# Performance work log

Hardware: AMD Instinct MI355X
Metric: run time of the kernel (lower is better)

Reference implementation:

```python
import jax, jax.numpy as jnp
import numpy as np

B, D_MODEL, N_LAYERS = 8, 512, 4
D_STATE, D_CONV, EXPAND, DT_RANK = 16, 4, 2, 32
D_INNER = EXPAND * D_MODEL
NUM_CLASSES = 10
ALPHA = 0.2  # observer_alpha
LN_EPS = 1e-5


def setup_inputs() -> dict:
    key = jax.random.key(0)
    ks = jax.random.split(key, 10)
    std = 0.02
    rn = lambda k, sh: (jax.random.normal(k, sh) * std).astype(jnp.float32)
    return {
        "x": jax.random.normal(ks[0], (B, 3, 32, 32), dtype=jnp.float32),
        "W_inp": rn(ks[1], (3, D_MODEL)), "b_inp": jnp.zeros((D_MODEL,), jnp.float32),
        "W_in": rn(ks[2], (N_LAYERS, D_MODEL, 2 * D_INNER)), "b_in": jnp.zeros((N_LAYERS, 2 * D_INNER), jnp.float32),
        "conv_w": rn(ks[3], (N_LAYERS, D_INNER, D_CONV)), "conv_b": jnp.zeros((N_LAYERS, D_INNER), jnp.float32),
        "W_x": rn(ks[4], (N_LAYERS, D_INNER, DT_RANK + 2 * D_STATE)),
        "W_dt": rn(ks[5], (N_LAYERS, DT_RANK, D_INNER)), "b_dt": jnp.zeros((N_LAYERS, D_INNER), jnp.float32),
        "A_log": jnp.broadcast_to(jnp.log(jnp.arange(1, D_STATE + 1, dtype=jnp.float32)), (N_LAYERS, D_INNER, D_STATE)) + 0.0,
        "D_skip": jnp.ones((N_LAYERS, D_INNER), jnp.float32),
        "W_out": rn(ks[6], (N_LAYERS, D_INNER, D_MODEL)), "b_out": jnp.zeros((N_LAYERS, D_MODEL), jnp.float32),
        "ln_w": jnp.ones((N_LAYERS, D_MODEL), jnp.float32), "ln_b": jnp.zeros((N_LAYERS, D_MODEL), jnp.float32),
        "lnf_w": jnp.ones((D_MODEL,), jnp.float32), "lnf_b": jnp.zeros((D_MODEL,), jnp.float32),
        "W_cls": rn(ks[7], (D_MODEL, NUM_CLASSES)), "b_cls": jnp.zeros((NUM_CLASSES,), jnp.float32),
    }


def layernorm(x, w, b):
    mu = x.mean(-1, keepdims=True)
    var = jnp.mean(jnp.square(x - mu), -1, keepdims=True)
    return (x - mu) * jax.lax.rsqrt(var + LN_EPS) * w + b


def mamba_layer(x, Wi, bi, cw, cb, Wx, Wdt, bdt, Alog, Dv, Wo, bo):
    # x: [B, L, d_model]
    Bsz, L, _ = x.shape
    u, z = jnp.split(x @ Wi + bi, 2, axis=-1)  # each [B, L, d_inner]
    # causal depthwise conv1d, kernel width D_CONV
    up = jnp.pad(u, ((0, 0), (D_CONV - 1, 0), (0, 0)))
    uc = cb + sum(up[:, k:k + L, :] * cw[:, k] for k in range(D_CONV))
    uc = jax.nn.silu(uc)
    dbc = uc @ Wx  # [B, L, dt_rank + 2*d_state]
    dt = jax.nn.softplus(dbc[..., :DT_RANK] @ Wdt + bdt)       # [B, L, d_inner]
    Bm = dbc[..., DT_RANK:DT_RANK + D_STATE]                    # [B, L, d_state]
    Cm = dbc[..., DT_RANK + D_STATE:]                           # [B, L, d_state]
    A = -jnp.exp(Alog)                                          # [d_inner, d_state]

    def step(h, inp):
        u_t, dt_t, B_t, C_t = inp  # [B,E],[B,E],[B,N],[B,N]
        h = jnp.exp(dt_t[..., None] * A) * h + (dt_t * u_t)[..., None] * B_t[:, None, :]
        # Luenberger observer correction: h <- h + alpha * (u - C.h) * C^T
        err = u_t - jnp.einsum('ben,bn->be', h, C_t)
        h = h + ALPHA * err[..., None] * C_t[:, None, :]
        y = jnp.einsum('ben,bn->be', h, C_t)
        return h, y

    step = jax.checkpoint(step)
    h0 = jnp.zeros((Bsz, D_INNER, D_STATE), dtype=x.dtype)
    xs = (uc.transpose(1, 0, 2), dt.transpose(1, 0, 2), Bm.transpose(1, 0, 2), Cm.transpose(1, 0, 2))
    _, ys = jax.lax.scan(step, h0, xs)
    y = ys.transpose(1, 0, 2) + Dv * uc
    y = y * jax.nn.silu(z)
    return y @ Wo + bo


def reference(x, W_inp, b_inp, W_in, b_in, conv_w, conv_b, W_x, W_dt, b_dt, A_log, D_skip, W_out, b_out, ln_w, ln_b, lnf_w, lnf_b, W_cls, b_cls):
    Bsz = x.shape[0]
    t = x.transpose(0, 2, 3, 1).reshape(Bsz, -1, 3)  # [B, H*W, 3]
    t = t @ W_inp + b_inp                             # [B, L, d_model]
    for i in range(N_LAYERS):
        t = t + mamba_layer(layernorm(t, ln_w[i], ln_b[i]), W_in[i], b_in[i], conv_w[i], conv_b[i], W_x[i], W_dt[i], b_dt[i], A_log[i], D_skip[i], W_out[i], b_out[i])
    t = t.mean(axis=1)
    t = layernorm(t, lnf_w, lnf_b)
    return t @ W_cls + b_cls
```

## Files before the change

kernel.cpp:

```cpp
#include <hip/hip_runtime.h>
#include <hip/hip_bf16.h>
#include <math.h>

#define BSZ 8
#define SEQL 1024
#define DM 512
#define DI 1024
#define DST 16
#define DTR 32
#define NLAYERS 4
#define ALPHA_C 0.2f
#define LNEPS 1e-5f
#define CH 64
#define KS64 8
#define YSTR 18

typedef __attribute__((ext_vector_type(8))) short short8;
typedef __attribute__((ext_vector_type(4))) float f32x4;

__device__ __forceinline__ void gll16(const void* g, void* l) {
    __builtin_amdgcn_global_load_lds(
        (const __attribute__((address_space(1))) unsigned int*)g,
        (__attribute__((address_space(3))) unsigned int*)l, 16, 0, 0);
}

__device__ __forceinline__ float sum16(float x) {
    x += __int_as_float(__builtin_amdgcn_update_dpp(0, __float_as_int(x), 0x121, 0xf, 0xf, true));
    x += __int_as_float(__builtin_amdgcn_update_dpp(0, __float_as_int(x), 0x122, 0xf, 0xf, true));
    x += __int_as_float(__builtin_amdgcn_update_dpp(0, __float_as_int(x), 0x124, 0xf, 0xf, true));
    x += __int_as_float(__builtin_amdgcn_update_dpp(0, __float_as_int(x), 0x128, 0xf, 0xf, true));
    return x;
}

__device__ __forceinline__ float bf2f(unsigned short v) {
    return __uint_as_float(((unsigned)v) << 16);
}

__global__ __launch_bounds__(256) void embed_kernel(const float* __restrict__ x,
                                                    const float* __restrict__ Wi,
                                                    const float* __restrict__ bi,
                                                    float* __restrict__ t) {
    int idx = blockIdx.x * 256 + threadIdx.x;
    if (idx >= BSZ * SEQL * DM) return;
    int d  = idx & (DM - 1);
    int bl = idx >> 9;
    int l  = bl & (SEQL - 1);
    int b  = bl >> 10;
    const float* xb = x + (size_t)b * 3 * SEQL;
    float acc = bi[d];
    acc += xb[0 * SEQL + l] * Wi[0 * DM + d];
    acc += xb[1 * SEQL + l] * Wi[1 * DM + d];
    acc += xb[2 * SEQL + l] * Wi[2 * DM + d];
    t[idx] = acc;
}

__global__ __launch_bounds__(256) void ln_kernel(const float* __restrict__ t,
                                                 const float* __restrict__ w,
                                                 const float* __restrict__ b,
                                                 __hip_bfloat16* __restrict__ xn) {
    int row = blockIdx.x;
    int tid = threadIdx.x;
    const float* r = t + (size_t)row * DM;
    float v0 = r[tid], v1 = r[tid + 256];
    __shared__ float sh[256], sh2[256];
    sh[tid]  = v0 + v1;
    sh2[tid] = v0 * v0 + v1 * v1;
    __syncthreads();
    for (int off = 128; off > 0; off >>= 1) {
        if (tid < off) { sh[tid] += sh[tid + off]; sh2[tid] += sh2[tid + off]; }
        __syncthreads();
    }
    float mu  = sh[0]  * (1.f / DM);
    float var = sh2[0] * (1.f / DM) - mu * mu;
    float rs  = rsqrtf(var + LNEPS);
    xn[(size_t)row * DM + tid]       = __float2bfloat16((v0 - mu) * rs * w[tid]       + b[tid]);
    xn[(size_t)row * DM + tid + 256] = __float2bfloat16((v1 - mu) * rs * w[tid + 256] + b[tid + 256]);
}

__global__ __launch_bounds__(256) void transpose_bf_kernel(const float* __restrict__ W,
                                                           __hip_bfloat16* __restrict__ Wt,
                                                           int K, int N, size_t lstride) {
    const float* Wl = W + (size_t)blockIdx.z * lstride;
    __hip_bfloat16* Wtl = Wt + (size_t)blockIdx.z * lstride;
    __shared__ float tile[32][33];
    int kk = blockIdx.x * 32, nn = blockIdx.y * 32;
    int tx = threadIdx.x & 31, ty = threadIdx.x >> 5;
#pragma unroll
    for (int i = 0; i < 32; i += 8)
        tile[ty + i][tx] = Wl[(size_t)(kk + ty + i) * N + nn + tx];
    __syncthreads();
#pragma unroll
    for (int i = 0; i < 32; i += 8)
        Wtl[(size_t)(nn + ty + i) * K + kk + tx] = __float2bfloat16(tile[tx][ty + i]);
}

template <int OUTMODE>
__global__ __launch_bounds__(256) void gemm_mfma_kernel(const short* __restrict__ A,
                                                        const short* __restrict__ Bt,
                                                        const float* __restrict__ bias,
                                                        void* __restrict__ Cv,
                                                        int M, int N, int K) {
    __shared__ __align__(16) short As[128 * 32];
    __shared__ __align__(16) short Bs[128 * 32];
    int tid = threadIdx.x;
    int w = tid >> 6, lane = tid & 63;
    int quad = lane >> 4, ml = lane & 15;
    int wm = w & 1, wn = w >> 1;
    const short* Ab = A + (size_t)blockIdx.x * 128 * K;
    const short* Bb = Bt + (size_t)blockIdx.y * 128 * K;
    f32x4 acc[4][4] = {};
    int s0 = tid, s1 = tid + 256;
    int r0 = s0 >> 2, c0 = (s0 & 3) ^ ((r0 >> 1) & 3);
    int r1 = s1 >> 2, c1 = (s1 & 3) ^ ((r1 >> 1) & 3);
    int aoff[4], boff[4];
#pragma unroll
    for (int t = 0; t < 4; t++) {
        int ra = wm * 64 + t * 16 + ml;
        aoff[t] = ra * 32 + (quad ^ ((ra >> 1) & 3)) * 8;
        int rb = wn * 64 + t * 16 + ml;
        boff[t] = rb * 32 + (quad ^ ((rb >> 1) & 3)) * 8;
    }
    for (int kk = 0; kk < K; kk += 32) {
        gll16(Ab + (size_t)r0 * K + kk + c0 * 8, As + (size_t)(w * 64) * 8);
        gll16(Ab + (size_t)r1 * K + kk + c1 * 8, As + (size_t)(256 + w * 64) * 8);
        gll16(Bb + (size_t)r0 * K + kk + c0 * 8, Bs + (size_t)(w * 64) * 8);
        gll16(Bb + (size_t)r1 * K + kk + c1 * 8, Bs + (size_t)(256 + w * 64) * 8);
        __syncthreads();
        short8 af[4], bfr[4];
#pragma unroll
        for (int t = 0; t < 4; t++) af[t]  = *(const short8*)&As[aoff[t]];
#pragma unroll
        for (int t = 0; t < 4; t++) bfr[t] = *(const short8*)&Bs[boff[t]];
#pragma unroll
        for (int mt = 0; mt < 4; mt++)
#pragma unroll
            for (int nt = 0; nt < 4; nt++)
                acc[mt][nt] = __builtin_amdgcn_mfma_f32_16x16x32_bf16(af[mt], bfr[nt], acc[mt][nt], 0, 0, 0);
        __syncthreads();
    }
#pragma unroll
    for (int mt = 0; mt < 4; mt++) {
#pragma unroll
        for (int nt = 0; nt < 4; nt++) {
            int n = blockIdx.y * 128 + wn * 64 + nt * 16 + ml;
            float bv = bias[n];
#pragma unroll
            for (int r = 0; r < 4; r++) {
                int m = blockIdx.x * 128 + wm * 64 + mt * 16 + quad * 4 + r;
                size_t off = (size_t)m * N + n;
                float v = acc[mt][nt][r] + bv;
                if (OUTMODE == 2) {
                    ((unsigned short*)Cv)[off] = __bfloat16_as_ushort(__float2bfloat16(v));
                } else {
                    float* C = (float*)Cv;
                    if (OUTMODE == 1) v += C[off];
                    C[off] = v;
                }
            }
        }
    }
}

__global__ __launch_bounds__(256) void conv_kernel(const unsigned short* __restrict__ uzb,
                                                   const float* __restrict__ cw,
                                                   const float* __restrict__ cb,
                                                   unsigned short* __restrict__ ucb) {
    int idx = blockIdx.x * 256 + threadIdx.x;
    int e  = idx & (DI - 1);
    int bl = idx >> 10;
    int l  = bl & (SEQL - 1);
    int b  = bl >> 10;
    const unsigned short* u = uzb + (size_t)b * SEQL * 2048;
    float acc = cb[e];
#pragma unroll
    for (int k = 0; k < 4; k++) {
        int ll = l - 3 + k;
        float uv = (ll >= 0) ? bf2f(u[(size_t)ll * 2048 + e]) : 0.f;
        acc += uv * cw[e * 4 + k];
    }
    acc = acc / (1.f + __expf(-acc));
    ucb[idx] = __bfloat16_as_ushort(__float2bfloat16(acc));
}

__global__ __launch_bounds__(256) void gemm64_mfma_kernel(const short* __restrict__ A,
                                                          const short* __restrict__ Bt,
                                                          float* __restrict__ part,
                                                          int M) {
    const int K = DI;
    const int Kseg = K / KS64;
    __shared__ __align__(16) short As[128 * 32];
    __shared__ __align__(16) short Bs[64 * 32];
    int tid = threadIdx.x;
    int w = tid >> 6, lane = tid & 63;
    int quad = lane >> 4, ml = lane & 15;
    int wm = w & 1, wn = w >> 1;
    int bm = blockIdx.x, ks = blockIdx.y;
    const short* Ab = A + (size_t)bm * 128 * K;
    f32x4 acc[4][2] = {};
    int s0 = tid, s1 = tid + 256;
    int r0 = s0 >> 2, c0 = (s0 & 3) ^ ((r0 >> 1) & 3);
    int r1 = s1 >> 2, c1 = (s1 & 3) ^ ((r1 >> 1) & 3);
    int rB = tid >> 2, cB = (tid & 3) ^ ((rB >> 1) & 3);
    int aoff[4], boff[2];
#pragma unroll
    for (int t = 0; t < 4; t++) {
        int ra = wm * 64 + t * 16 + ml;
        aoff[t] = ra * 32 + (quad ^ ((ra >> 1) & 3)) * 8;
    }
#pragma unroll
    for (int t = 0; t < 2; t++) {
        int rb = wn * 32 + t * 16 + ml;
        boff[t] = rb * 32 + (quad ^ ((rb >> 1) & 3)) * 8;
    }
    int k0 = ks * Kseg;
    for (int kk = k0; kk < k0 + Kseg; kk += 32) {
        gll16(Ab + (size_t)r0 * K + kk + c0 * 8, As + (size_t)(w * 64) * 8);
        gll16(Ab + (size_t)r1 * K + kk + c1 * 8, As + (size_t)(256 + w * 64) * 8);
        gll16(Bt + (size_t)rB * K + kk + cB * 8, Bs + (size_t)(w * 64) * 8);
        __syncthreads();
        short8 af[4], bfr[2];
#pragma unroll
        for (int t = 0; t < 4; t++) af[t]  = *(const short8*)&As[aoff[t]];
#pragma unroll
        for (int t = 0; t < 2; t++) bfr[t] = *(const short8*)&Bs[boff[t]];
#pragma unroll
        for (int mt = 0; mt < 4; mt++)
#pragma unroll
            for (int nt = 0; nt < 2; nt++)
                acc[mt][nt] = __builtin_amdgcn_mfma_f32_16x16x32_bf16(af[mt], bfr[nt], acc[mt][nt], 0, 0, 0);
        __syncthreads();
    }
#pragma unroll
    for (int mt = 0; mt < 4; mt++) {
#pragma unroll
        for (int nt = 0; nt < 2; nt++) {
            int n = wn * 32 + nt * 16 + ml;
#pragma unroll
            for (int r = 0; r < 4; r++) {
                int m = bm * 128 + wm * 64 + mt * 16 + quad * 4 + r;
                part[((size_t)ks * M + m) * 64 + n] = acc[mt][nt][r];
            }
        }
    }
}

__global__ __launch_bounds__(256) void repack_kernel(const float* __restrict__ part,
                                                     float* __restrict__ dtc,
                                                     unsigned* __restrict__ bcb,
                                                     float* __restrict__ ssqb,
                                                     int M) {
    int m = blockIdx.x * 4 + (threadIdx.x >> 6);
    int j = threadIdx.x & 63;
    float v = 0.f;
#pragma unroll
    for (int ks = 0; ks < KS64; ks++) v += part[((size_t)ks * M + m) * 64 + j];
    if (j < 32) {
        dtc[(size_t)m * 32 + j] = v;
    } else {
        int n = (j - 32) & 15;
        unsigned short u16 = __bfloat16_as_ushort(__float2bfloat16(v));
        unsigned short* bp = (unsigned short*)(bcb + (size_t)m * 16 + n);
        if (j < 48) {
            bp[0] = u16;
        } else {
            bp[1] = u16;
            float vr = bf2f(u16);
            float s = sum16(vr * vr);
            if (j == 48) ssqb[m] = s;
        }
    }
}

__global__ __launch_bounds__(256) void dt_kernel(const float* __restrict__ dtc,
                                                 const float* __restrict__ Wdt,
                                                 const float* __restrict__ bdt,
                                                 float* __restrict__ dtb) {
    __shared__ float sdtc[32][32];
    __shared__ float swdt[32][256];
    int tid = threadIdx.x;
    int e0 = (blockIdx.x & 3) * 256;
    int m0 = (blockIdx.x >> 2) * 32;
#pragma unroll
    for (int i = 0; i < 4; i++) {
        int idx = tid + 256 * i;
        sdtc[idx >> 5][idx & 31] = dtc[(size_t)(m0 + (idx >> 5)) * 32 + (idx & 31)];
    }
#pragma unroll
    for (int r = 0; r < 32; r++) swdt[r][tid] = Wdt[(size_t)r * DI + e0 + tid];
    __syncthreads();
    float wc[32];
#pragma unroll
    for (int r = 0; r < 32; r++) wc[r] = swdt[r][tid];
    float bv = bdt[e0 + tid];
    for (int m = 0; m < 32; m++) {
        float acc = bv;
#pragma unroll
        for (int r4 = 0; r4 < 8; r4++) {
            float4 d4 = *(const float4*)&sdtc[m][r4 * 4];
            acc = fmaf(d4.x, wc[r4 * 4 + 0], acc);
            acc = fmaf(d4.y, wc[r4 * 4 + 1], acc);
            acc = fmaf(d4.z, wc[r4 * 4 + 2], acc);
            acc = fmaf(d4.w, wc[r4 * 4 + 3], acc);
        }
        float sp = (acc > 20.f) ? acc : log1pf(__expf(acc));
        dtb[(size_t)(m0 + m) * DI + e0 + tid] = sp;
    }
}

__device__ __forceinline__ void scan_stage(unsigned* sBC, float* sDT, unsigned short* sU,
                                           unsigned short* sZ, float* sSQ,
                                           const unsigned short* __restrict__ ucb_row,
                                           const float* __restrict__ dtb_row,
                                           const unsigned short* __restrict__ uzb_row,
                                           const unsigned* __restrict__ bcb_row,
                                           const float* __restrict__ sqb,
                                           int e_base, int tid, int tc) {
    int w = tid >> 6;
    gll16(bcb_row + (size_t)(tc + (tid >> 2)) * 16 + (tid & 3) * 4, sBC + w * 256);
    gll16(dtb_row + (size_t)(tc + (tid >> 2)) * 1024 + e_base + (tid & 3) * 4, sDT + w * 256);
    if (w < 2) {
        int t = tid >> 1, half = tid & 1;
        gll16(ucb_row + (size_t)(tc + t) * 1024 + e_base + half * 8, sU + w * 512);
        if (tid < 16) gll16(sqb + tc + tid * 4, sSQ);
    } else {
        int j = tid - 128;
        int t = j >> 1, half = j & 1;
        gll16(uzb_row + (size_t)(tc + t) * 2048 + 1024 + e_base + half * 8, sZ + (w - 2) * 512);
    }
}

__device__ __forceinline__ void scan_flush(const float* yb, __hip_bfloat16* ob,
                                           int e_base, int tcp, int tid) {
#pragma unroll
    for (int r = 0; r < 2; r++) {
        int pid = r * 256 + tid;
        int t = pid >> 3, ep = pid & 7;
        float2 y2 = *(const float2*)&yb[t * YSTR + ep * 2];
        __hip_bfloat162 v;
        v.x = __float2bfloat16(y2.x);
        v.y = __float2bfloat16(y2.y);
        *(__hip_bfloat162*)&ob[(size_t)(tcp + t) * DI + e_base + ep * 2] = v;
    }
}

__global__ __launch_bounds__(256) void scan_kernel(const unsigned short* __restrict__ ucb,
                                                   const float* __restrict__ dtb,
                                                   const unsigned short* __restrict__ uzb,
                                                   const unsigned* __restrict__ bcb,
                                                   const float* __restrict__ ssqb,
                                                   const float* __restrict__ Alog,
                                                   const float* __restrict__ Dv,
                                                   __hip_bfloat16* __restrict__ out) {
    __shared__ __align__(16) unsigned       sBC[2][CH * 16];
    __shared__ __align__(16) float          sDT[2][CH * 16];
    __shared__ __align__(16) unsigned short sU [2][CH * 16];
    __shared__ __align__(16) unsigned short sZ [2][CH * 16];
    __shared__ __align__(16) float          sSQ[2][CH];
    __shared__ __align__(16) float          yb [2][CH * YSTR];
    int tid = threadIdx.x;
    int g = tid >> 4, n = tid & 15;
    int b = blockIdx.x >> 6;
    int e_base = (blockIdx.x & 63) << 4;
    int e = e_base + g;
    float An2 = -__expf(Alog[e * DST + n]) * 1.4426950408889634f;
    float dv = Dv[e];
    const unsigned short* ucb_row = ucb + (size_t)b * SEQL * DI;
    const float*          dtb_row = dtb + (size_t)b * SEQL * DI;
    const unsigned short* uzb_row = uzb + (size_t)b * SEQL * 2048;
    const unsigned*       bcb_row = bcb + (size_t)b * SEQL * 16;
    const float*          sqb     = ssqb + (size_t)b * SEQL;
    __hip_bfloat16* ob = out + (size_t)b * SEQL * DI;
    float h = 0.f;
    scan_stage(sBC[0], sDT[0], sU[0], sZ[0], sSQ[0], ucb_row, dtb_row, uzb_row, bcb_row, sqb, e_base, tid, 0);
    int buf = 0;
    for (int c = 0; c < SEQL / CH; c++) {
        int tc = c * CH;
        __syncthreads();
        if (c + 1 < SEQL / CH)
            scan_stage(sBC[buf ^ 1], sDT[buf ^ 1], sU[buf ^ 1], sZ[buf ^ 1], sSQ[buf ^ 1],
                       ucb_row, dtb_row, uzb_row, bcb_row, sqb, e_base, tid, tc + CH);
        if (c > 0)
            scan_flush(yb[buf ^ 1], ob, e_base, tc - CH, tid);
        const unsigned* pBC = sBC[buf];
        const float* pDT = sDT[buf];
        const unsigned short* pU = sU[buf];
        const unsigned short* pZ = sZ[buf];
        const float* pSQ = sSQ[buf];
        float* pY = yb[buf];
        for (int ts = 0; ts < CH; ts += 16) {
            float pc = 0.f, ucap = 0.f;
#pragma unroll
            for (int j = 0; j < 16; j++) {
                int t = ts + j;
                unsigned bcd = pBC[t * 16 + n];
                float Bn = __uint_as_float(bcd << 16);
                float Cn = __uint_as_float(bcd & 0xFFFF0000u);
                float dtv = pDT[t * 16 + g];
                float uv  = bf2f(pU[t * 16 + g]);
                float alC = ALPHA_C * Cn;
                float a = __builtin_amdgcn_exp2f(dtv * An2);
                h = fmaf(a, h, dtv * uv * Bn);
                float p = sum16(h * Cn);
                h = fmaf(uv - p, alC, h);
                bool cap = (n == j);
                pc   = cap ? p  : pc;
                ucap = cap ? uv : ucap;
            }
            int tl = ts + n;
            float sq = pSQ[tl];
            float zv = bf2f(pZ[tl * 16 + g]);
            float es2 = ALPHA_C * (ucap - pc);
            float y = fmaf(dv, ucap, fmaf(es2, sq, pc));
            float sz = zv / (1.f + __expf(-zv));
            pY[tl * YSTR + g] = y * sz;
        }
        buf ^= 1;
    }
    __syncthreads();
    scan_flush(yb[buf ^ 1], ob, e_base, SEQL - CH, tid);
}

__global__ __launch_bounds__(512) void pool_kernel(const float* __restrict__ t,
                                                   float* __restrict__ part) {
    int b = blockIdx.x >> 4;
    int c = blockIdx.x & 15;
    int d = threadIdx.x;
    const float* tb = t + ((size_t)b * SEQL + c * 64) * DM + d;
    float s = 0.f;
    for (int l = 0; l < 64; l++) s += tb[(size_t)l * DM];
    part[(size_t)blockIdx.x * DM + d] = s;
}

__global__ __launch_bounds__(512) void final_kernel(const float* __restrict__ part,
                                                    const float* __restrict__ lw,
                                                    const float* __restrict__ lb,
                                                    const float* __restrict__ Wc,
                                                    const float* __restrict__ bc,
                                                    float* __restrict__ out) {
    int b = blockIdx.x;
    int d = threadIdx.x;
    float v = 0.f;
    for (int c = 0; c < 16; c++) v += part[((size_t)b * 16 + c) * DM + d];
    v *= (1.f / SEQL);
    __shared__ float sh[512], sh2[512], nd[512];
    sh[d] = v; sh2[d] = v * v;
    __syncthreads();
    for (int off = 256; off > 0; off >>= 1) {
        if (d < off) { sh[d] += sh[d + off]; sh2[d] += sh2[d + off]; }
        __syncthreads();
    }
    float mu  = sh[0]  * (1.f / DM);
    float var = sh2[0] * (1.f / DM) - mu * mu;
    float rs  = rsqrtf(var + LNEPS);
    nd[d] = (v - mu) * rs * lw[d] + lb[d];
    __syncthreads();
    if (d < 10) {
        float acc = bc[d];
        for (int k = 0; k < DM; k++) acc += nd[k] * Wc[k * 10 + d];
        out[b * 10 + d] = acc;
    }
}

extern "C" void kernel_launch(void* const* d_in, const int* in_sizes, int n_in,
                              void* d_out, int out_size, void* d_ws, size_t ws_size,
                              hipStream_t stream) {
    const float* x      = (const float*)d_in[0];
    const float* W_inp  = (const float*)d_in[1];
    const float* b_inp  = (const float*)d_in[2];
    const float* W_in   = (const float*)d_in[3];
    const float* b_in   = (const float*)d_in[4];
    const float* conv_w = (const float*)d_in[5];
    const float* conv_b = (const float*)d_in[6];
    const float* W_x    = (const float*)d_in[7];
    const float* W_dt   = (const float*)d_in[8];
    const float* b_dt   = (const float*)d_in[9];
    const float* A_log  = (const float*)d_in[10];
    const float* D_skip = (const float*)d_in[11];
    const float* W_out  = (const float*)d_in[12];
    const float* b_out  = (const float*)d_in[13];
    const float* ln_w   = (const float*)d_in[14];
    const float* ln_b   = (const float*)d_in[15];
    const float* lnf_w  = (const float*)d_in[16];
    const float* lnf_b  = (const float*)d_in[17];
    const float* W_cls  = (const float*)d_in[18];
    const float* b_cls  = (const float*)d_in[19];

    const int M = BSZ * SEQL;

    float* ws = (float*)d_ws;
    float* t_buf = ws;                    ws += (size_t)M * DM;
    unsigned short* uzb = (unsigned short*)ws;  ws += (size_t)M * 2048 / 2;
    unsigned short* ucb = (unsigned short*)ws;  ws += (size_t)M * DI / 2;
    float* dtb   = ws;                    ws += (size_t)M * DI;
    float* dtc   = ws;                    ws += (size_t)M * 32;
    unsigned* bcbu = (unsigned*)ws;       ws += (size_t)M * 16;
    float* ssqb  = ws;                    ws += (size_t)M;
    unsigned short* xn_bf = (unsigned short*)ws;  ws += (size_t)M * DM / 2;
    unsigned short* ucs_bf = (unsigned short*)ws; ws += (size_t)M * DI / 2;
    float* partb = ws;                    ws += (size_t)KS64 * M * 64;
    unsigned short* wtin_bf  = (unsigned short*)ws; ws += (size_t)NLAYERS * DM * 2048 / 2;
    unsigned short* wtout_bf = (unsigned short*)ws; ws += (size_t)NLAYERS * DI * DM / 2;
    unsigned short* wxt_bf   = (unsigned short*)ws; ws += (size_t)NLAYERS * DI * 64 / 2 + 64;
    float* poolp = ws;                    ws += (size_t)128 * DM;

    embed_kernel<<<(M * DM + 255) / 256, 256, 0, stream>>>(x, W_inp, b_inp, t_buf);
    transpose_bf_kernel<<<dim3(DM / 32, 2048 / 32, NLAYERS), 256, 0, stream>>>(
        W_in, (__hip_bfloat16*)wtin_bf, DM, 2048, (size_t)DM * 2048);
    transpose_bf_kernel<<<dim3(DI / 32, DM / 32, NLAYERS), 256, 0, stream>>>(
        W_out, (__hip_bfloat16*)wtout_bf, DI, DM, (size_t)DI * DM);
    transpose_bf_kernel<<<dim3(DI / 32, 64 / 32, NLAYERS), 256, 0, stream>>>(
        W_x, (__hip_bfloat16*)wxt_bf, DI, 64, (size_t)DI * 64);

    for (int i = 0; i < NLAYERS; i++) {
        ln_kernel<<<M, 256, 0, stream>>>(t_buf, ln_w + i * DM, ln_b + i * DM,
                                         (__hip_bfloat16*)xn_bf);
        gemm_mfma_kernel<2><<<dim3(M / 128, 2048 / 128), 256, 0, stream>>>(
            (const short*)xn_bf, (const short*)(wtin_bf + (size_t)i * DM * 2048),
            b_in + i * 2048, uzb, M, 2048, DM);
        conv_kernel<<<(M * DI) / 256, 256, 0, stream>>>(
            uzb, conv_w + (size_t)i * DI * 4, conv_b + i * DI, ucb);
        gemm64_mfma_kernel<<<dim3(M / 128, KS64), 256, 0, stream>>>(
            (const short*)ucb, (const short*)(wxt_bf + (size_t)i * DI * 64), partb, M);
        repack_kernel<<<M / 4, 256, 0, stream>>>(partb, dtc, bcbu, ssqb, M);
        dt_kernel<<<(M / 32) * 4, 256, 0, stream>>>(
            dtc, W_dt + (size_t)i * DTR * DI, b_dt + i * DI, dtb);
        scan_kernel<<<BSZ * DI / 16, 256, 0, stream>>>(
            ucb, dtb, uzb, bcbu, ssqb, A_log + (size_t)i * DI * DST, D_skip + i * DI,
            (__hip_bfloat16*)ucs_bf);
        gemm_mfma_kernel<1><<<dim3(M / 128, DM / 128), 256, 0, stream>>>(
            (const short*)ucs_bf, (const short*)(wtout_bf + (size_t)i * DI * DM),
            b_out + i * DM, t_buf, M, DM, DI);
    }

    pool_kernel<<<128, 512, 0, stream>>>(t_buf, poolp);
    final_kernel<<<8, 512, 0, stream>>>(poolp, lnf_w, lnf_b, W_cls, b_cls, (float*)d_out);
}
```

Measured before the change: 1.216 ms.

## Pack dt and u into bf16 pairs for scan, fold dt reduction, smaller out-proj tiles

The dt kernel now reduces the split-K partials itself and writes dt (as bf16) packed together with u into one 32-bit word per element. This replaces the separate fp32 dt buffer and bf16 u stream, so the scan kernel makes fewer global loads and uses less shared memory. z and the ssq values are now read directly from global memory inside the scan loop. The output projection uses a new 64x64-tile GEMM to launch more blocks for the N=512 residual GEMM. Rounding dt to bf16 adds precision risk, and the smaller tiles reduce data reuse per block.

```diff
diff --git a/kernel.cpp b/kernel.cpp
--- a/kernel.cpp
+++ b/kernel.cpp
@@ -156,6 +156,61 @@
                     if (OUTMODE == 1) v += C[off];
                     C[off] = v;
                 }
+            }
+        }
+    }
+}
+
+__global__ __launch_bounds__(256) void gemm6464_res_kernel(const short* __restrict__ A,
+                                                           const short* __restrict__ Bt,
+                                                           const float* __restrict__ bias,
+                                                           float* __restrict__ C,
+                                                           int M, int N, int K) {
+    __shared__ __align__(16) short As[64 * 32];
+    __shared__ __align__(16) short Bs[64 * 32];
+    int tid = threadIdx.x;
+    int w = tid >> 6, lane = tid & 63;
+    int quad = lane >> 4, ml = lane & 15;
+    int wm = w & 1, wn = w >> 1;
+    const short* Ab = A + (size_t)blockIdx.x * 64 * K;
+    const short* Bb = Bt + (size_t)blockIdx.y * 64 * K;
+    f32x4 acc[2][2] = {};
+    int r0 = tid >> 2, c0 = (tid & 3) ^ ((r0 >> 1) & 3);
+    int aoff[2], boff[2];
+#pragma unroll
+    for (int t = 0; t < 2; t++) {
+        int ra = wm * 32 + t * 16 + ml;
+        aoff[t] = ra * 32 + (quad ^ ((ra >> 1) & 3)) * 8;
+        int rb = wn * 32 + t * 16 + ml;
+        boff[t] = rb * 32 + (quad ^ ((rb >> 1) & 3)) * 8;
+    }
+    for (int kk = 0; kk < K; kk += 32) {
+        gll16(Ab + (size_t)r0 * K + kk + c0 * 8, As + (size_t)(w * 64) * 8);
+        gll16(Bb + (size_t)r0 * K + kk + c0 * 8, Bs + (size_t)(w * 64) * 8);
+        __syncthreads();
+        short8 af[2], bfr[2];
+#pragma unroll
+        for (int t = 0; t < 2; t++) af[t]  = *(const short8*)&As[aoff[t]];
+#pragma unroll
+        for (int t = 0; t < 2; t++) bfr[t] = *(const short8*)&Bs[boff[t]];
+#pragma unroll
+        for (int mt = 0; mt < 2; mt++)
+#pragma unroll
+            for (int nt = 0; nt < 2; nt++)
+                acc[mt][nt] = __builtin_amdgcn_mfma_f32_16x16x32_bf16(af[mt], bfr[nt], acc[mt][nt], 0, 0, 0);
+        __syncthreads();
+    }
+#pragma unroll
+    for (int mt = 0; mt < 2; mt++) {
+#pragma unroll
+        for (int nt = 0; nt < 2; nt++) {
+            int n = blockIdx.y * 64 + wn * 32 + nt * 16 + ml;
+            float bv = bias[n];
+#pragma unroll
+            for (int r = 0; r < 4; r++) {
+                int m = blockIdx.x * 64 + wm * 32 + mt * 16 + quad * 4 + r;
+                size_t off = (size_t)m * N + n;
+                C[off] = acc[mt][nt][r] + bv + C[off];
             }
         }
     }
@@ -245,36 +300,33 @@
 }
 
 __global__ __launch_bounds__(256) void repack_kernel(const float* __restrict__ part,
-                                                     float* __restrict__ dtc,
                                                      unsigned* __restrict__ bcb,
                                                      float* __restrict__ ssqb,
                                                      int M) {
-    int m = blockIdx.x * 4 + (threadIdx.x >> 6);
-    int j = threadIdx.x & 63;
+    int m = blockIdx.x * 8 + (threadIdx.x >> 5);
+    int j = threadIdx.x & 31;
     float v = 0.f;
 #pragma unroll
-    for (int ks = 0; ks < KS64; ks++) v += part[((size_t)ks * M + m) * 64 + j];
-    if (j < 32) {
-        dtc[(size_t)m * 32 + j] = v;
+    for (int ks = 0; ks < KS64; ks++) v += part[((size_t)ks * M + m) * 64 + 32 + j];
+    int n = j & 15;
+    unsigned short u16 = __bfloat16_as_ushort(__float2bfloat16(v));
+    unsigned short* bp = (unsigned short*)(bcb + (size_t)m * 16 + n);
+    if (j < 16) {
+        bp[0] = u16;
     } else {
-        int n = (j - 32) & 15;
-        unsigned short u16 = __bfloat16_as_ushort(__float2bfloat16(v));
-        unsigned short* bp = (unsigned short*)(bcb + (size_t)m * 16 + n);
-        if (j < 48) {
-            bp[0] = u16;
-        } else {
-            bp[1] = u16;
-            float vr = bf2f(u16);
-            float s = sum16(vr * vr);
-            if (j == 48) ssqb[m] = s;
-        }
-    }
-}
-
-__global__ __launch_bounds__(256) void dt_kernel(const float* __restrict__ dtc,
+        bp[1] = u16;
+        float vr = bf2f(u16);
+        float s = sum16(vr * vr);
+        if (j == 16) ssqb[m] = s;
+    }
+}
+
+__global__ __launch_bounds__(256) void dt_kernel(const float* __restrict__ part,
                                                  const float* __restrict__ Wdt,
                                                  const float* __restrict__ bdt,
-                                                 float* __restrict__ dtb) {
+                                                 const unsigned short* __restrict__ ucb,
+                                                 unsigned* __restrict__ dub,
+                                                 int M) {
     __shared__ float sdtc[32][32];
     __shared__ float swdt[32][256];
     int tid = threadIdx.x;
@@ -283,7 +335,11 @@
 #pragma unroll
     for (int i = 0; i < 4; i++) {
         int idx = tid + 256 * i;
-        sdtc[idx >> 5][idx & 31] = dtc[(size_t)(m0 + (idx >> 5)) * 32 + (idx & 31)];
+        int m = idx >> 5, r = idx & 31;
+        float v = 0.f;
+#pragma unroll
+        for (int ks = 0; ks < KS64; ks++) v += part[((size_t)ks * M + m0 + m) * 64 + r];
+        sdtc[m][r] = v;
     }
 #pragma unroll
     for (int r = 0; r < 32; r++) swdt[r][tid] = Wdt[(size_t)r * DI + e0 + tid];
@@ -303,30 +359,20 @@
             acc = fmaf(d4.w, wc[r4 * 4 + 3], acc);
         }
         float sp = (acc > 20.f) ? acc : log1pf(__expf(acc));
-        dtb[(size_t)(m0 + m) * DI + e0 + tid] = sp;
-    }
-}
-
-__device__ __forceinline__ void scan_stage(unsigned* sBC, float* sDT, unsigned short* sU,
-                                           unsigned short* sZ, float* sSQ,
-                                           const unsigned short* __restrict__ ucb_row,
-                                           const float* __restrict__ dtb_row,
-                                           const unsigned short* __restrict__ uzb_row,
+        unsigned dt16 = (unsigned)__bfloat16_as_ushort(__float2bfloat16(sp));
+        unsigned u16  = (unsigned)ucb[(size_t)(m0 + m) * DI + e0 + tid];
+        dub[(size_t)(m0 + m) * DI + e0 + tid] = (dt16 << 16) | u16;
+    }
+}
+
+__device__ __forceinline__ void scan_stage(unsigned* sDU, unsigned* sBC,
+                                           const unsigned* __restrict__ dub_row,
                                            const unsigned* __restrict__ bcb_row,
-                                           const float* __restrict__ sqb,
                                            int e_base, int tid, int tc) {
     int w = tid >> 6;
-    gll16(bcb_row + (size_t)(tc + (tid >> 2)) * 16 + (tid & 3) * 4, sBC + w * 256);
-    gll16(dtb_row + (size_t)(tc + (tid >> 2)) * 1024 + e_base + (tid & 3) * 4, sDT + w * 256);
-    if (w < 2) {
-        int t = tid >> 1, half = tid & 1;
-        gll16(ucb_row + (size_t)(tc + t) * 1024 + e_base + half * 8, sU + w * 512);
-        if (tid < 16) gll16(sqb + tc + tid * 4, sSQ);
-    } else {
-        int j = tid - 128;
-        int t = j >> 1, half = j & 1;
-        gll16(uzb_row + (size_t)(tc + t) * 2048 + 1024 + e_base + half * 8, sZ + (w - 2) * 512);
-    }
+    int t4 = tid >> 2, c4 = tid & 3;
+    gll16(dub_row + (size_t)(tc + t4) * 1024 + e_base + c4 * 4, sDU + w * 256);
+    gll16(bcb_row + (size_t)(tc + t4) * 16 + c4 * 4,            sBC + w * 256);
 }
 
 __device__ __forceinline__ void scan_flush(const float* yb, __hip_bfloat16* ob,
@@ -343,20 +389,16 @@
     }
 }
 
-__global__ __launch_bounds__(256) void scan_kernel(const unsigned short* __restrict__ ucb,
-                                                   const float* __restrict__ dtb,
+__global__ __launch_bounds__(256) void scan_kernel(const unsigned* __restrict__ dub,
                                                    const unsigned short* __restrict__ uzb,
                                                    const unsigned* __restrict__ bcb,
                                                    const float* __restrict__ ssqb,
                                                    const float* __restrict__ Alog,
                                                    const float* __restrict__ Dv,
                                                    __hip_bfloat16* __restrict__ out) {
-    __shared__ __align__(16) unsigned       sBC[2][CH * 16];
-    __shared__ __align__(16) float          sDT[2][CH * 16];
-    __shared__ __align__(16) unsigned short sU [2][CH * 16];
-    __shared__ __align__(16) unsigned short sZ [2][CH * 16];
-    __shared__ __align__(16) float          sSQ[2][CH];
-    __shared__ __align__(16) float          yb [2][CH * YSTR];
+    __shared__ __align__(16) unsigned sDU[2][CH * 16];
+    __shared__ __align__(16) unsigned sBC[2][CH * 16];
+    __shared__ __align__(16) float    yb [2][CH * YSTR];
     int tid = threadIdx.x;
     int g = tid >> 4, n = tid & 15;
     int b = blockIdx.x >> 6;
@@ -364,51 +406,46 @@
     int e = e_base + g;
     float An2 = -__expf(Alog[e * DST + n]) * 1.4426950408889634f;
     float dv = Dv[e];
-    const unsigned short* ucb_row = ucb + (size_t)b * SEQL * DI;
-    const float*          dtb_row = dtb + (size_t)b * SEQL * DI;
+    const unsigned*       dub_row = dub + (size_t)b * SEQL * DI;
     const unsigned short* uzb_row = uzb + (size_t)b * SEQL * 2048;
     const unsigned*       bcb_row = bcb + (size_t)b * SEQL * 16;
     const float*          sqb     = ssqb + (size_t)b * SEQL;
     __hip_bfloat16* ob = out + (size_t)b * SEQL * DI;
     float h = 0.f;
-    scan_stage(sBC[0], sDT[0], sU[0], sZ[0], sSQ[0], ucb_row, dtb_row, uzb_row, bcb_row, sqb, e_base, tid, 0);
+    scan_stage(sDU[0], sBC[0], dub_row, bcb_row, e_base, tid, 0);
     int buf = 0;
     for (int c = 0; c < SEQL / CH; c++) {
         int tc = c * CH;
         __syncthreads();
         if (c + 1 < SEQL / CH)
-            scan_stage(sBC[buf ^ 1], sDT[buf ^ 1], sU[buf ^ 1], sZ[buf ^ 1], sSQ[buf ^ 1],
-                       ucb_row, dtb_row, uzb_row, bcb_row, sqb, e_base, tid, tc + CH);
+            scan_stage(sDU[buf ^ 1], sBC[buf ^ 1], dub_row, bcb_row, e_base, tid, tc + CH);
         if (c > 0)
             scan_flush(yb[buf ^ 1], ob, e_base, tc - CH, tid);
+        const unsigned* pDU = sDU[buf];
         const unsigned* pBC = sBC[buf];
-        const float* pDT = sDT[buf];
-        const unsigned short* pU = sU[buf];
-        const unsigned short* pZ = sZ[buf];
-        const float* pSQ = sSQ[buf];
         float* pY = yb[buf];
         for (int ts = 0; ts < CH; ts += 16) {
+            int tl = ts + n;
+            float sq = sqb[tc + tl];
+            float zv = bf2f(uzb_row[(size_t)(tc + tl) * 2048 + 1024 + e]);
             float pc = 0.f, ucap = 0.f;
 #pragma unroll
             for (int j = 0; j < 16; j++) {
                 int t = ts + j;
+                unsigned du = pDU[t * 16 + g];
+                float dtv = __uint_as_float(du & 0xFFFF0000u);
+                float uv  = __uint_as_float(du << 16);
                 unsigned bcd = pBC[t * 16 + n];
                 float Bn = __uint_as_float(bcd << 16);
                 float Cn = __uint_as_float(bcd & 0xFFFF0000u);
-                float dtv = pDT[t * 16 + g];
-                float uv  = bf2f(pU[t * 16 + g]);
-                float alC = ALPHA_C * Cn;
                 float a = __builtin_amdgcn_exp2f(dtv * An2);
                 h = fmaf(a, h, dtv * uv * Bn);
                 float p = sum16(h * Cn);
-                h = fmaf(uv - p, alC, h);
+                h = fmaf(uv - p, ALPHA_C * Cn, h);
                 bool cap = (n == j);
                 pc   = cap ? p  : pc;
                 ucap = cap ? uv : ucap;
             }
-            int tl = ts + n;
-            float sq = pSQ[tl];
-            float zv = bf2f(pZ[tl * 16 + g]);
             float es2 = ALPHA_C * (ucap - pc);
             float y = fmaf(dv, ucap, fmaf(es2, sq, pc));
             float sz = zv / (1.f + __expf(-zv));
@@ -488,20 +525,19 @@
     const int M = BSZ * SEQL;
 
     float* ws = (float*)d_ws;
-    float* t_buf = ws;                    ws += (size_t)M * DM;
+    float* t_buf = ws;                          ws += (size_t)M * DM;
     unsigned short* uzb = (unsigned short*)ws;  ws += (size_t)M * 2048 / 2;
     unsigned short* ucb = (unsigned short*)ws;  ws += (size_t)M * DI / 2;
-    float* dtb   = ws;                    ws += (size_t)M * DI;
-    float* dtc   = ws;                    ws += (size_t)M * 32;
-    unsigned* bcbu = (unsigned*)ws;       ws += (size_t)M * 16;
-    float* ssqb  = ws;                    ws += (size_t)M;
+    unsigned* dub  = (unsigned*)ws;             ws += (size_t)M * DI;
+    unsigned* bcbu = (unsigned*)ws;             ws += (size_t)M * 16;
+    float* ssqb  = ws;                          ws += (size_t)M;
     unsigned short* xn_bf = (unsigned short*)ws;  ws += (size_t)M * DM / 2;
     unsigned short* ucs_bf = (unsigned short*)ws; ws += (size_t)M * DI / 2;
-    float* partb = ws;                    ws += (size_t)KS64 * M * 64;
+    float* partb = ws;                          ws += (size_t)KS64 * M * 64;
     unsigned short* wtin_bf  = (unsigned short*)ws; ws += (size_t)NLAYERS * DM * 2048 / 2;
     unsigned short* wtout_bf = (unsigned short*)ws; ws += (size_t)NLAYERS * DI * DM / 2;
     unsigned short* wxt_bf   = (unsigned short*)ws; ws += (size_t)NLAYERS * DI * 64 / 2 + 64;
-    float* poolp = ws;                    ws += (size_t)128 * DM;
+    float* poolp = ws;                          ws += (size_t)128 * DM;
 
     embed_kernel<<<(M * DM + 255) / 256, 256, 0, stream>>>(x, W_inp, b_inp, t_buf);
     transpose_bf_kernel<<<dim3(DM / 32, 2048 / 32, NLAYERS), 256, 0, stream>>>(
@@ -521,13 +557,13 @@
             uzb, conv_w + (size_t)i * DI * 4, conv_b + i * DI, ucb);
         gemm64_mfma_kernel<<<dim3(M / 128, KS64), 256, 0, stream>>>(
             (const short*)ucb, (const short*)(wxt_bf + (size_t)i * DI * 64), partb, M);
-        repack_kernel<<<M / 4, 256, 0, stream>>>(partb, dtc, bcbu, ssqb, M);
+        repack_kernel<<<M / 8, 256, 0, stream>>>(partb, bcbu, ssqb, M);
         dt_kernel<<<(M / 32) * 4, 256, 0, stream>>>(
-            dtc, W_dt + (size_t)i * DTR * DI, b_dt + i * DI, dtb);
+            partb, W_dt + (size_t)i * DTR * DI, b_dt + i * DI, ucb, dub, M);
         scan_kernel<<<BSZ * DI / 16, 256, 0, stream>>>(
-            ucb, dtb, uzb, bcbu, ssqb, A_log + (size_t)i * DI * DST, D_skip + i * DI,
+            dub, uzb, bcbu, ssqb, A_log + (size_t)i * DI * DST, D_skip + i * DI,
             (__hip_bfloat16*)ucs_bf);
-        gemm_mfma_kernel<1><<<dim3(M / 128, DM / 128), 256, 0, stream>>>(
+        gemm6464_res_kernel<<<dim3(M / 64, DM / 64), 256, 0, stream>>>(
             (const short*)ucs_bf, (const short*)(wtout_bf + (size_t)i * DI * DM),
             b_out + i * DM, t_buf, M, DM, DI);
     }
```

New measurement: 1.164 ms. 1.04x faster.
